# Kernel tuning notes

Hardware: AMD Instinct MI355X
Metric: run time of the kernel (lower is better)

Reference implementation:

```python
import jax, jax.numpy as jnp
import numpy as np

B, S, E, H = 4, 1024, 768, 8
HD = E // H
FF = 4 * E
SCALING = HD ** -0.5


def _layernorm(x, g, b, eps=1e-5):
    m = jnp.mean(x, axis=-1, keepdims=True)
    v = jnp.var(x, axis=-1, keepdims=True)
    return (x - m) / jnp.sqrt(v + eps) * g + b


def setup_inputs() -> dict:
    key = jax.random.key(0)
    ks = jax.random.split(key, 12)
    w = lambda k, shp: (jax.random.normal(k, shp, jnp.float32) * 0.02)
    return {
        "x": jax.random.normal(ks[0], (B, S, E), jnp.float32),
        "dist_map": jax.random.uniform(ks[1], (B, H, S, S), jnp.float32),
        "mask": jnp.zeros((B, S), jnp.int32),
        "Wq": w(ks[2], (E, E)), "bq": jnp.zeros((E,), jnp.float32),
        "Wk": w(ks[3], (E, E)), "bk": jnp.zeros((E,), jnp.float32),
        "Wv": w(ks[4], (E, E)), "bv": jnp.zeros((E,), jnp.float32),
        "Wo": w(ks[5], (E, E)), "bo": jnp.zeros((E,), jnp.float32),
        "ln1_g": jnp.ones((E,), jnp.float32), "ln1_b": jnp.zeros((E,), jnp.float32),
        "W1": w(ks[6], (FF, E)), "b1": jnp.zeros((FF,), jnp.float32),
        "W2": w(ks[7], (E, FF)), "b2": jnp.zeros((E,), jnp.float32),
        "ln2_g": jnp.ones((E,), jnp.float32), "ln2_b": jnp.zeros((E,), jnp.float32),
    }


def reference(x, dist_map, mask, Wq, bq, Wk, bk, Wv, bv, Wo, bo,
              ln1_g, ln1_b, W1, b1, W2, b2, ln2_g, ln2_b):
    # --- attention residual block (pre-norm) ---
    h = _layernorm(x, ln1_g, ln1_b)
    # NOTE: torch does .view(B, H, S, HD) directly on [B, S, E] -> pure reshape, no transpose
    q = (h @ Wq.T + bq).reshape(B, H, S, HD)
    k = (h @ Wk.T + bk).reshape(B, H, S, HD)
    v = (h @ Wv.T + bv).reshape(B, H, S, HD)
    attn_weights = jnp.einsum("bhqd,bhkd->bhqk", q, k)
    pad = mask.astype(bool)[:, None, None, :]          # [B,1,1,S]
    attn_weights = jnp.where(pad, -10000.0, attn_weights)  # mask BEFORE scaling (as in source)
    probs = jax.nn.softmax(attn_weights * SCALING, axis=-1)
    probs = (probs + dist_map) * 0.5                   # post-softmax dist bias
    ctx = jnp.einsum("bhal,bhlv->bhav", probs, v)      # [B,H,S,HD]
    ctx = ctx.transpose(0, 2, 1, 3).reshape(B, S, E)
    x1 = x + (ctx @ Wo.T + bo)
    # --- FFN residual block (pre-norm) ---
    h2 = _layernorm(x1, ln2_g, ln2_b)
    ffn = jax.nn.gelu(h2 @ W1.T + b1, approximate=False) @ W2.T + b2
    out = x1 + ffn
    return out, probs
```

## Files before the change

kernel.cpp:

```cpp
#include <hip/hip_runtime.h>
#include <math.h>

typedef unsigned short u16;
typedef u16   u16x8  __attribute__((ext_vector_type(8)));
typedef u16   u16x4  __attribute__((ext_vector_type(4)));
typedef __bf16 bf16x8 __attribute__((ext_vector_type(8)));
typedef float f32x4  __attribute__((ext_vector_type(4)));

#define SZ_BSE   3145728
#define HEADSZ   98304
#define SCALING  0.10206207261596577f

__device__ __forceinline__ u16 f2bf(float f) {
  union { float f; unsigned u; } c; c.f = f;
  unsigned u = c.u;
  return (u16)((u + 0x7fffu + ((u >> 16) & 1u)) >> 16);
}
__device__ __forceinline__ float bf2f(u16 v) {
  union { unsigned u; float f; } c; c.u = ((unsigned)v) << 16; return c.f;
}

typedef const __attribute__((address_space(1))) unsigned int* gas1_t;
typedef __attribute__((address_space(3))) unsigned int* las3_t;
__device__ __forceinline__ void gload16(const void* g, void* l) {
  __builtin_amdgcn_global_load_lds((gas1_t)g, (las3_t)l, 16, 0, 0);
}

struct CvtArgs {
  const float* src[6];
  u16* dst[6];
};
__global__ __launch_bounds__(256) void cvtall_k(CvtArgs a) {
  int bid = blockIdx.x;
  int which, base;
  if (bid < 2304)      { which = bid / 576; base = (bid - which * 576) * 1024; }
  else if (bid < 4608) { which = 4; base = (bid - 2304) * 1024; }
  else                 { which = 5; base = (bid - 4608) * 1024; }
  int i = base + threadIdx.x * 4;
  f32x4 v = *(const f32x4*)&a.src[which][i];
  u16x4 o; o[0]=f2bf(v[0]); o[1]=f2bf(v[1]); o[2]=f2bf(v[2]); o[3]=f2bf(v[3]);
  *(u16x4*)&a.dst[which][i] = o;
}

__global__ __launch_bounds__(256) void ln_k(const float* __restrict__ x,
                                            const float* __restrict__ g,
                                            const float* __restrict__ b,
                                            u16* __restrict__ out) {
  const int row = blockIdx.x;
  const float* xr = x + (long)row * 768;
  const int t = threadIdx.x;
  float v0 = xr[t], v1 = xr[t + 256], v2 = xr[t + 512];
  float s = v0 + v1 + v2, ss = v0*v0 + v1*v1 + v2*v2;
  for (int o = 32; o > 0; o >>= 1) { s += __shfl_xor(s, o); ss += __shfl_xor(ss, o); }
  __shared__ float red[8];
  int w = t >> 6;
  if ((t & 63) == 0) { red[w] = s; red[w + 4] = ss; }
  __syncthreads();
  s  = red[0] + red[1] + red[2] + red[3];
  ss = red[4] + red[5] + red[6] + red[7];
  float mean = s * (1.0f / 768.0f);
  float var  = ss * (1.0f / 768.0f) - mean * mean;
  float rstd = rsqrtf(var + 1e-5f);
  u16* orow = out + (long)row * 768;
  orow[t]       = f2bf((v0 - mean) * rstd * g[t]       + b[t]);
  orow[t + 256] = f2bf((v1 - mean) * rstd * g[t + 256] + b[t + 256]);
  orow[t + 512] = f2bf((v2 - mean) * rstd * g[t + 512] + b[t + 512]);
}

__global__ __launch_bounds__(256) void reduce_k(const float* __restrict__ p,
                                                const float* __restrict__ resid,
                                                const float* __restrict__ bias,
                                                float* __restrict__ out) {
  long i = ((long)blockIdx.x * 256 + threadIdx.x) * 4;
  f32x4 a = *(const f32x4*)&p[i];
  f32x4 b = *(const f32x4*)&p[3145728 + i];
  f32x4 c = *(const f32x4*)&p[6291456 + i];
  f32x4 r = *(const f32x4*)&resid[i];
  int cb = (int)(i % 768);
  f32x4 g = *(const f32x4*)&bias[cb];
  f32x4 o;
  o[0] = r[0] + g[0] + a[0] + b[0] + c[0];
  o[1] = r[1] + g[1] + a[1] + b[1] + c[1];
  o[2] = r[2] + g[2] + a[2] + b[2] + c[2];
  o[3] = r[3] + g[3] + a[3] + b[3] + c[3];
  *(f32x4*)&out[i] = o;
}

__global__ __launch_bounds__(512, 4)
void scores_k(const u16* __restrict__ qb, const u16* __restrict__ kb,
              const int* __restrict__ maskp, float* __restrict__ probs,
              float* __restrict__ rowsInv) {
  __shared__ float sSum[2][64];
  __shared__ u16 sFlag[1024];

  const int t = threadIdx.x;
  const int z = blockIdx.y;
  const int r0 = blockIdx.x * 64;
  const int b = z >> 3;

  {
    const int* mp = maskp + b * 1024 + t * 2;
    int2 mv = *(const int2*)mp;
    sFlag[t * 2]     = (u16)(mv.x != 0);
    sFlag[t * 2 + 1] = (u16)(mv.y != 0);
  }
  __syncthreads();

  const int lane = t & 63;
  const int w = t >> 6;
  const int rs = w & 3, ch = w >> 2;
  const int wr0 = rs * 16;
  const int lr = lane & 15, lg = lane >> 4;
  const int cbase = ch * 512;

  const u16* qh = qb + (long)z * HEADSZ;
  const u16* kh = kb + (long)z * HEADSZ;
  float* ph = probs + (long)z * 1048576;

  bf16x8 qa[3];
  {
    const u16* qr = qh + (long)(r0 + wr0 + lr) * 96 + lg * 8;
#pragma unroll
    for (int kf = 0; kf < 3; ++kf) qa[kf] = *(const bf16x8*)(qr + kf * 32);
  }

  const float neg = -10000.0f * SCALING;
  float srun[4] = {0.f, 0.f, 0.f, 0.f};

  for (int c = 0; c < 8; ++c) {
    const int c0 = cbase + c * 64;
    f32x4 a4[4] = {};
#pragma unroll
    for (int ni = 0; ni < 4; ++ni) {
      const u16* kr = kh + (long)(c0 + ni * 16 + lr) * 96 + lg * 8;
#pragma unroll
      for (int kf = 0; kf < 3; ++kf)
        a4[ni] = __builtin_amdgcn_mfma_f32_16x16x32_bf16(
            qa[kf], *(const bf16x8*)(kr + kf * 32), a4[ni], 0, 0, 0);
    }
#pragma unroll
    for (int ni = 0; ni < 4; ++ni) {
      bool fm = sFlag[c0 + ni * 16 + lr] != 0;
      float* pp = ph + (long)(r0 + wr0 + lg * 4) * 1024 + c0 + ni * 16 + lr;
#pragma unroll
      for (int r = 0; r < 4; ++r) {
        float sv = fm ? neg : a4[ni][r] * SCALING;
        float e = __expf(sv);
        srun[r] += e;
        pp[r * 1024] = e;
      }
    }
  }

#pragma unroll
  for (int r = 0; r < 4; ++r) {
    float s = srun[r];
    s += __shfl_xor(s, 1);
    s += __shfl_xor(s, 2);
    s += __shfl_xor(s, 4);
    s += __shfl_xor(s, 8);
    if (lr == 0) sSum[ch][wr0 + lg * 4 + r] = s;
  }
  __syncthreads();
  if (ch == 0 && lr == 0) {
#pragma unroll
    for (int r = 0; r < 4; ++r) {
      float iv = 1.0f / (sSum[0][wr0 + lg * 4 + r] + sSum[1][wr0 + lg * 4 + r]);
      rowsInv[(long)z * 1024 + r0 + wr0 + lg * 4 + r] = iv;
    }
  }
}

__global__ __launch_bounds__(512, 2)
void pv2_k(float* __restrict__ probs, const float* __restrict__ dist,
           const float* __restrict__ rowsInv, const u16* __restrict__ vT,
           u16* __restrict__ ctx) {
  __shared__ u16 sP[8 * 16 * 72];
  __shared__ float sX[4 * 64 * 24];

  const int t = threadIdx.x;
  const int z = blockIdx.y;
  const int r0 = blockIdx.x * 64;
  const int b = z >> 3, h = z & 7;
  const int lane = t & 63, w = t >> 6;
  const int rs = w & 3, ch = w >> 2;
  const int wr0 = rs * 16;
  const int lr = lane & 15, lg = lane >> 4;
  const int cbase = ch * 512;
  const int lrow = lane >> 2;
  const int cg = (lane & 3) * 16;
  u16* sPw = sP + w * (16 * 72);

  float* ph = probs + (long)z * 1048576;
  const float* dh = dist + (long)z * 1048576;
  const u16* vh = vT + (long)z * HEADSZ;
  const float iv = rowsInv[(long)z * 1024 + r0 + wr0 + lrow];

  f32x4 cacc[6] = {};
#pragma unroll
  for (int c = 0; c < 8; ++c) {
    const int c0 = cbase + c * 64;
    float* pp = ph + (long)(r0 + wr0 + lrow) * 1024 + c0 + cg;
    const float* dp = dh + (long)(r0 + wr0 + lrow) * 1024 + c0 + cg;
    f32x4 e0 = *(const f32x4*)pp;
    f32x4 e1 = *(const f32x4*)(pp + 4);
    f32x4 e2 = *(const f32x4*)(pp + 8);
    f32x4 e3 = *(const f32x4*)(pp + 12);
    f32x4 d0 = *(const f32x4*)dp;
    f32x4 d1 = *(const f32x4*)(dp + 4);
    f32x4 d2 = *(const f32x4*)(dp + 8);
    f32x4 d3 = *(const f32x4*)(dp + 12);
    f32x4 p0, p1, p2, p3;
#pragma unroll
    for (int j = 0; j < 4; ++j) {
      p0[j] = (e0[j] * iv + d0[j]) * 0.5f;
      p1[j] = (e1[j] * iv + d1[j]) * 0.5f;
      p2[j] = (e2[j] * iv + d2[j]) * 0.5f;
      p3[j] = (e3[j] * iv + d3[j]) * 0.5f;
    }
    *(f32x4*)pp        = p0;
    *(f32x4*)(pp + 4)  = p1;
    *(f32x4*)(pp + 8)  = p2;
    *(f32x4*)(pp + 12) = p3;
    u16x8 o0, o1;
#pragma unroll
    for (int j = 0; j < 4; ++j) {
      o0[j] = f2bf(p0[j]); o0[4 + j] = f2bf(p1[j]);
      o1[j] = f2bf(p2[j]); o1[4 + j] = f2bf(p3[j]);
    }
    *(u16x8*)&sPw[lrow * 72 + cg]     = o0;
    *(u16x8*)&sPw[lrow * 72 + cg + 8] = o1;

#pragma unroll
    for (int ks = 0; ks < 2; ++ks) {
      bf16x8 pa = *(const bf16x8*)&sPw[lr * 72 + ks * 32 + lg * 8];
      const u16* vr = vh + (long)lr * 1024 + c0 + ks * 32 + lg * 8;
#pragma unroll
      for (int n2 = 0; n2 < 6; ++n2) {
        bf16x8 vb = *(const bf16x8*)(vr + (long)n2 * 16384);
        cacc[n2] = __builtin_amdgcn_mfma_f32_16x16x32_bf16(pa, vb, cacc[n2], 0, 0, 0);
      }
    }
  }

  __syncthreads();
  if (ch == 1) {
    float* xp = sX + ((rs * 64 + lane) * 24);
#pragma unroll
    for (int n2 = 0; n2 < 6; ++n2) *(f32x4*)&xp[n2 * 4] = cacc[n2];
  }
  __syncthreads();
  if (ch == 0) {
    const float* xp = sX + ((rs * 64 + lane) * 24);
    u16* cbp = ctx + (long)b * 786432 + h * 96;
#pragma unroll
    for (int n2 = 0; n2 < 6; ++n2) {
      f32x4 xv = *(const f32x4*)&xp[n2 * 4];
      int d = n2 * 16 + lr;
#pragma unroll
      for (int r = 0; r < 4; ++r)
        cbp[(long)(r0 + wr0 + lg * 4 + r) * 768 + d] = f2bf(cacc[n2][r] + xv[r]);
    }
  }
}

enum { EPI_QKV = 0, EPI_GELU = 1, EPI_PARTIAL = 2 };

template <int EPI>
__global__ __launch_bounds__(256, 2)
void gemm_k(const u16* __restrict__ A, int lda,
            const u16* __restrict__ W, int ldw,
            void* __restrict__ Cv, long sCz, int ldc,
            const float* __restrict__ bias,
            u16* __restrict__ vt,
            int N, int K, int kchunks) {
  __shared__ u16 sA[4096];
  __shared__ u16 sB[4096];

  const int t  = threadIdx.x;
  const int kc = blockIdx.z;
  const int klen = K / kchunks;
  const int kbeg = kc * klen, kend = kbeg + klen;
  const int m0 = blockIdx.x * 128;
  const int n0 = blockIdx.y * 128;

  const int r0 = t >> 2;
  const int c0 = (t & 3) << 3;
  char* lA = (char*)sA + ((t >> 6) << 10);
  char* lB = (char*)sB + ((t >> 6) << 10);

  int bn0 = n0 + r0;      if (bn0 > N - 1) bn0 = N - 1;
  int bn1 = n0 + 64 + r0; if (bn1 > N - 1) bn1 = N - 1;
  const u16* gB0 = W + (long)bn0 * ldw + c0;
  const u16* gB1 = W + (long)bn1 * ldw + c0;
  const u16* gA0 = A + (long)(m0 + r0) * lda + c0;
  const u16* gA1 = gA0 + 64 * lda;

  const int lane = t & 63;
  const int w  = t >> 6;
  const int wm = (w >> 1) * 64, wn = (w & 1) * 64;
  const int lr = lane & 15, lg = lane >> 4;

  f32x4 acc[4][4] = {};

  for (int k0 = kbeg; k0 < kend; k0 += 32) {
    gload16(gA0 + k0, lA);
    gload16(gA1 + k0, lA + 4096);
    gload16(gB0 + k0, lB);
    gload16(gB1 + k0, lB + 4096);
    __syncthreads();

    bf16x8 aF[4], bF[4];
#pragma unroll
    for (int mi = 0; mi < 4; ++mi)
      aF[mi] = *(const bf16x8*)&sA[(wm + mi * 16 + lr) * 32 + lg * 8];
#pragma unroll
    for (int ni = 0; ni < 4; ++ni)
      bF[ni] = *(const bf16x8*)&sB[(wn + ni * 16 + lr) * 32 + lg * 8];
#pragma unroll
    for (int mi = 0; mi < 4; ++mi)
#pragma unroll
      for (int ni = 0; ni < 4; ++ni)
        acc[mi][ni] = __builtin_amdgcn_mfma_f32_16x16x32_bf16(aF[mi], bF[ni], acc[mi][ni], 0, 0, 0);
    __syncthreads();
  }

  long coff = (EPI == EPI_PARTIAL) ? (long)kc * sCz : 0;

#pragma unroll
  for (int mi = 0; mi < 4; ++mi) {
#pragma unroll
    for (int ni = 0; ni < 4; ++ni) {
      int gc = n0 + wn + ni * 16 + lr;
      if (gc >= N) continue;
      int gr0 = m0 + wm + mi * 16 + lg * 4;
#pragma unroll
      for (int r = 0; r < 4; ++r) {
        float vv = acc[mi][ni][r];
        if (EPI == EPI_QKV) {
          vv += bias[gc];
          if (gc >= 1536) {
            int c = gc - 1536;
            int row = gr0 + r, bb = row >> 10, sr = row & 1023;
            int hh = sr >> 7;
            int cd = c / 96;
            int ss = ((sr & 127) << 3) + cd;
            int dd = c - cd * 96;
            vt[(long)(bb * 8 + hh) * HEADSZ + (long)dd * 1024 + ss] = f2bf(vv);
          } else {
            int wsel = gc >= 768 ? 1 : 0;
            int c = gc - wsel * 768;
            ((u16*)Cv)[(long)wsel * 3145728 + (long)(gr0 + r) * 768 + c] = f2bf(vv);
          }
        } else if (EPI == EPI_GELU) {
          vv += bias[gc];
          vv = 0.5f * vv * (1.0f + erff(vv * 0.70710678118654752f));
          ((u16*)Cv)[coff + (long)(gr0 + r) * ldc + gc] = f2bf(vv);
        } else {
          ((float*)Cv)[coff + (long)(gr0 + r) * ldc + gc] = vv;
        }
      }
    }
  }
}

extern "C" void kernel_launch(void* const* d_in, const int* in_sizes, int n_in,
                              void* d_out, int out_size, void* d_ws, size_t ws_size,
                              hipStream_t stream) {
  (void)in_sizes; (void)n_in; (void)out_size; (void)ws_size;
  const float* x    = (const float*)d_in[0];
  const float* dist = (const float*)d_in[1];
  const int*   mask = (const int*)d_in[2];
  const float* Wq = (const float*)d_in[3];  const float* bq  = (const float*)d_in[4];
  const float* Wk = (const float*)d_in[5];  const float* bk  = (const float*)d_in[6];
  const float* Wv = (const float*)d_in[7];  const float* bv  = (const float*)d_in[8];
  const float* Wo = (const float*)d_in[9];  const float* bo  = (const float*)d_in[10];
  const float* g1 = (const float*)d_in[11]; const float* b1n = (const float*)d_in[12];
  const float* W1 = (const float*)d_in[13]; const float* b1f = (const float*)d_in[14];
  const float* W2 = (const float*)d_in[15]; const float* b2f = (const float*)d_in[16];
  const float* g2 = (const float*)d_in[17]; const float* b2n = (const float*)d_in[18];

  char* ws = (char*)d_ws;
  u16*   h    = (u16*)(ws + 0);
  u16*   ctx  = (u16*)(ws + 0);
  u16*   qk   = (u16*)(ws + 6291456);
  u16*   q    = qk;
  u16*   k    = (u16*)(ws + 12582912);
  u16*   vT   = (u16*)(ws + 25165824);
  float* part = (float*)(ws + 6291456);
  u16*   h2   = (u16*)(ws + 31457280);
  u16*   ffn1 = (u16*)(ws + 44040192);
  float* x1   = (float*)(ws + 69206016);
  u16*   wqkvb= (u16*)(ws + 81788928);
  u16*   wob  = (u16*)(ws + 85327872);
  u16*   w1b  = (u16*)(ws + 86507520);
  u16*   w2b  = (u16*)(ws + 91226112);
  float* bqkv = (float*)(ws + 95944704);
  float* rowsInv = (float*)(ws + 95953920);

  float* outp   = (float*)d_out;
  float* probs  = outp + SZ_BSE;

  CvtArgs ca;
  ca.src[0] = Wq; ca.src[1] = Wk; ca.src[2] = Wv;
  ca.src[3] = Wo; ca.src[4] = W1; ca.src[5] = W2;
  ca.dst[0] = wqkvb; ca.dst[1] = wqkvb + 589824; ca.dst[2] = wqkvb + 1179648;
  ca.dst[3] = wob;   ca.dst[4] = w1b;            ca.dst[5] = w2b;
  cvtall_k<<<6912, 256, 0, stream>>>(ca);
  hipMemcpyAsync(bqkv,        bq, 3072, hipMemcpyDeviceToDevice, stream);
  hipMemcpyAsync(bqkv + 768,  bk, 3072, hipMemcpyDeviceToDevice, stream);
  hipMemcpyAsync(bqkv + 1536, bv, 3072, hipMemcpyDeviceToDevice, stream);

  ln_k<<<4096, 256, 0, stream>>>(x, g1, b1n, h);

  gemm_k<EPI_QKV><<<dim3(32, 18, 1), 256, 0, stream>>>(
      h, 768, wqkvb, 768, qk, 0, 768, bqkv, vT, 2304, 768, 1);

  scores_k<<<dim3(16, 32), 512, 0, stream>>>(q, k, mask, probs, rowsInv);
  pv2_k<<<dim3(16, 32), 512, 0, stream>>>(probs, dist, rowsInv, vT, ctx);

  gemm_k<EPI_PARTIAL><<<dim3(32, 6, 3), 256, 0, stream>>>(
      ctx, 768, wob, 768, part, 3145728, 768, nullptr, nullptr, 768, 768, 3);
  reduce_k<<<3072, 256, 0, stream>>>(part, x, bo, x1);

  ln_k<<<4096, 256, 0, stream>>>(x1, g2, b2n, h2);

  gemm_k<EPI_GELU><<<dim3(32, 24, 1), 256, 0, stream>>>(
      h2, 768, w1b, 768, ffn1, 0, 3072, b1f, nullptr, 3072, 768, 1);

  gemm_k<EPI_PARTIAL><<<dim3(32, 6, 3), 256, 0, stream>>>(
      ffn1, 3072, w2b, 3072, part, 3145728, 768, nullptr, nullptr, 768, 3072, 3);
  reduce_k<<<3072, 256, 0, stream>>>(part, x1, b2f, outp);
}
```

Before: 341.7 us.

## Store bf16 exp scores, split probs finalize and PV, widen GEMM K-step

The scores kernel now writes unnormalized exponentials as bf16 into the upper half of each probs row, going through LDS so the global stores are coalesced. A new elementwise probs_k finalizes probs from those values and dist_map. A separate pv_k then rereads the fp32 probs and converts them to bf16 in registers before the MFMA. This is meant to cut the fp32 exp write and read traffic and to let pv_k run at higher occupancy without an LDS staging step. In exchange it adds an extra kernel launch and a second pass over probs. The GEMM now loads 64 K per barrier (double-size LDS tiles) to halve the syncs, and the N bounds clamps and checks are removed.

```diff
diff --git a/kernel.cpp b/kernel.cpp
--- a/kernel.cpp
+++ b/kernel.cpp
@@ -90,6 +90,7 @@
 void scores_k(const u16* __restrict__ qb, const u16* __restrict__ kb,
               const int* __restrict__ maskp, float* __restrict__ probs,
               float* __restrict__ rowsInv) {
+  __shared__ u16 sP[8 * 16 * 72];
   __shared__ float sSum[2][64];
   __shared__ u16 sFlag[1024];
 
@@ -112,10 +113,13 @@
   const int wr0 = rs * 16;
   const int lr = lane & 15, lg = lane >> 4;
   const int cbase = ch * 512;
+  u16* sPw = sP + w * (16 * 72);
+  const int lrow = lane >> 2;
+  const int cg = (lane & 3) * 16;
 
   const u16* qh = qb + (long)z * HEADSZ;
   const u16* kh = kb + (long)z * HEADSZ;
-  float* ph = probs + (long)z * 1048576;
+  u16* eb = (u16*)probs + (long)z * 2097152;
 
   bf16x8 qa[3];
   {
@@ -141,15 +145,19 @@
 #pragma unroll
     for (int ni = 0; ni < 4; ++ni) {
       bool fm = sFlag[c0 + ni * 16 + lr] != 0;
-      float* pp = ph + (long)(r0 + wr0 + lg * 4) * 1024 + c0 + ni * 16 + lr;
 #pragma unroll
       for (int r = 0; r < 4; ++r) {
         float sv = fm ? neg : a4[ni][r] * SCALING;
         float e = __expf(sv);
         srun[r] += e;
-        pp[r * 1024] = e;
+        sPw[(lg * 4 + r) * 72 + ni * 16 + lr] = f2bf(e);
       }
     }
+    u16x8 e0 = *(const u16x8*)&sPw[lrow * 72 + cg];
+    u16x8 e1 = *(const u16x8*)&sPw[lrow * 72 + cg + 8];
+    u16* ep = eb + (long)(r0 + wr0 + lrow) * 2048 + 1024 + c0 + cg;
+    *(u16x8*)ep       = e0;
+    *(u16x8*)(ep + 8) = e1;
   }
 
 #pragma unroll
@@ -171,86 +179,92 @@
   }
 }
 
-__global__ __launch_bounds__(512, 2)
-void pv2_k(float* __restrict__ probs, const float* __restrict__ dist,
-           const float* __restrict__ rowsInv, const u16* __restrict__ vT,
-           u16* __restrict__ ctx) {
-  __shared__ u16 sP[8 * 16 * 72];
+__global__ __launch_bounds__(256)
+void probs_k(float* __restrict__ probs, const float* __restrict__ dist,
+             const float* __restrict__ rowsInv) {
+  const long gidx = (long)blockIdx.x * 4 + (threadIdx.x >> 6);
+  const int l16 = (threadIdx.x & 63) * 16;
+  float* pr = probs + gidx * 1024 + l16;
+  const u16* er = (const u16*)(probs + gidx * 1024) + 1024 + l16;
+  const float* dr = dist + gidx * 1024 + l16;
+  const float iv = rowsInv[gidx];
+
+  u16x8 e0 = *(const u16x8*)er;
+  u16x8 e1 = *(const u16x8*)(er + 8);
+  f32x4 d0 = *(const f32x4*)dr;
+  f32x4 d1 = *(const f32x4*)(dr + 4);
+  f32x4 d2 = *(const f32x4*)(dr + 8);
+  f32x4 d3 = *(const f32x4*)(dr + 12);
+  __syncthreads();
+  f32x4 o0, o1, o2, o3;
+#pragma unroll
+  for (int j = 0; j < 4; ++j) {
+    o0[j] = (bf2f(e0[j])     * iv + d0[j]) * 0.5f;
+    o1[j] = (bf2f(e0[4 + j]) * iv + d1[j]) * 0.5f;
+    o2[j] = (bf2f(e1[j])     * iv + d2[j]) * 0.5f;
+    o3[j] = (bf2f(e1[4 + j]) * iv + d3[j]) * 0.5f;
+  }
+  *(f32x4*)pr        = o0;
+  *(f32x4*)(pr + 4)  = o1;
+  *(f32x4*)(pr + 8)  = o2;
+  *(f32x4*)(pr + 12) = o3;
+}
+
+__global__ __launch_bounds__(512, 4)
+void pv_k(const float* __restrict__ probs, const u16* __restrict__ vT,
+          u16* __restrict__ ctx) {
   __shared__ float sX[4 * 64 * 24];
-
   const int t = threadIdx.x;
   const int z = blockIdx.y;
   const int r0 = blockIdx.x * 64;
   const int b = z >> 3, h = z & 7;
   const int lane = t & 63, w = t >> 6;
-  const int rs = w & 3, ch = w >> 2;
+  const int rs = w & 3, kh = w >> 2;
   const int wr0 = rs * 16;
   const int lr = lane & 15, lg = lane >> 4;
-  const int cbase = ch * 512;
-  const int lrow = lane >> 2;
-  const int cg = (lane & 3) * 16;
-  u16* sPw = sP + w * (16 * 72);
-
-  float* ph = probs + (long)z * 1048576;
-  const float* dh = dist + (long)z * 1048576;
+
+  const float* ph = probs + (long)z * 1048576 + (long)(r0 + wr0 + lr) * 1024 + lg * 8;
   const u16* vh = vT + (long)z * HEADSZ;
-  const float iv = rowsInv[(long)z * 1024 + r0 + wr0 + lrow];
+  const int cb = kh * 512;
 
   f32x4 cacc[6] = {};
 #pragma unroll
   for (int c = 0; c < 8; ++c) {
-    const int c0 = cbase + c * 64;
-    float* pp = ph + (long)(r0 + wr0 + lrow) * 1024 + c0 + cg;
-    const float* dp = dh + (long)(r0 + wr0 + lrow) * 1024 + c0 + cg;
-    f32x4 e0 = *(const f32x4*)pp;
-    f32x4 e1 = *(const f32x4*)(pp + 4);
-    f32x4 e2 = *(const f32x4*)(pp + 8);
-    f32x4 e3 = *(const f32x4*)(pp + 12);
-    f32x4 d0 = *(const f32x4*)dp;
-    f32x4 d1 = *(const f32x4*)(dp + 4);
-    f32x4 d2 = *(const f32x4*)(dp + 8);
-    f32x4 d3 = *(const f32x4*)(dp + 12);
-    f32x4 p0, p1, p2, p3;
+    const int c0 = cb + c * 64;
+    const float* pp = ph + c0;
+    f32x4 p0 = *(const f32x4*)pp;
+    f32x4 p1 = *(const f32x4*)(pp + 4);
+    f32x4 p2 = *(const f32x4*)(pp + 32);
+    f32x4 p3 = *(const f32x4*)(pp + 36);
+    u16x8 w0, w1;
 #pragma unroll
     for (int j = 0; j < 4; ++j) {
-      p0[j] = (e0[j] * iv + d0[j]) * 0.5f;
-      p1[j] = (e1[j] * iv + d1[j]) * 0.5f;
-      p2[j] = (e2[j] * iv + d2[j]) * 0.5f;
-      p3[j] = (e3[j] * iv + d3[j]) * 0.5f;
-    }
-    *(f32x4*)pp        = p0;
-    *(f32x4*)(pp + 4)  = p1;
-    *(f32x4*)(pp + 8)  = p2;
-    *(f32x4*)(pp + 12) = p3;
-    u16x8 o0, o1;
-#pragma unroll
-    for (int j = 0; j < 4; ++j) {
-      o0[j] = f2bf(p0[j]); o0[4 + j] = f2bf(p1[j]);
-      o1[j] = f2bf(p2[j]); o1[4 + j] = f2bf(p3[j]);
-    }
-    *(u16x8*)&sPw[lrow * 72 + cg]     = o0;
-    *(u16x8*)&sPw[lrow * 72 + cg + 8] = o1;
-
-#pragma unroll
-    for (int ks = 0; ks < 2; ++ks) {
-      bf16x8 pa = *(const bf16x8*)&sPw[lr * 72 + ks * 32 + lg * 8];
-      const u16* vr = vh + (long)lr * 1024 + c0 + ks * 32 + lg * 8;
-#pragma unroll
-      for (int n2 = 0; n2 < 6; ++n2) {
-        bf16x8 vb = *(const bf16x8*)(vr + (long)n2 * 16384);
-        cacc[n2] = __builtin_amdgcn_mfma_f32_16x16x32_bf16(pa, vb, cacc[n2], 0, 0, 0);
-      }
-    }
-  }
-
-  __syncthreads();
-  if (ch == 1) {
+      w0[j] = f2bf(p0[j]); w0[4 + j] = f2bf(p1[j]);
+      w1[j] = f2bf(p2[j]); w1[4 + j] = f2bf(p3[j]);
+    }
+    bf16x8 pa0 = *(bf16x8*)&w0;
+    bf16x8 pa1 = *(bf16x8*)&w1;
+    const u16* vr0 = vh + (long)lr * 1024 + c0 + lg * 8;
+#pragma unroll
+    for (int n2 = 0; n2 < 6; ++n2) {
+      bf16x8 vb = *(const bf16x8*)(vr0 + (long)n2 * 16384);
+      cacc[n2] = __builtin_amdgcn_mfma_f32_16x16x32_bf16(pa0, vb, cacc[n2], 0, 0, 0);
+    }
+#pragma unroll
+    for (int n2 = 0; n2 < 6; ++n2) {
+      bf16x8 vb = *(const bf16x8*)(vr0 + 32 + (long)n2 * 16384);
+      cacc[n2] = __builtin_amdgcn_mfma_f32_16x16x32_bf16(pa1, vb, cacc[n2], 0, 0, 0);
+    }
+  }
+
+  __syncthreads();
+  if (kh == 1) {
     float* xp = sX + ((rs * 64 + lane) * 24);
 #pragma unroll
     for (int n2 = 0; n2 < 6; ++n2) *(f32x4*)&xp[n2 * 4] = cacc[n2];
   }
   __syncthreads();
-  if (ch == 0) {
+  if (kh == 0) {
     const float* xp = sX + ((rs * 64 + lane) * 24);
     u16* cbp = ctx + (long)b * 786432 + h * 96;
 #pragma unroll
@@ -274,8 +288,8 @@
             const float* __restrict__ bias,
             u16* __restrict__ vt,
             int N, int K, int kchunks) {
-  __shared__ u16 sA[4096];
-  __shared__ u16 sB[4096];
+  __shared__ u16 sA[8192];
+  __shared__ u16 sB[8192];
 
   const int t  = threadIdx.x;
   const int kc = blockIdx.z;
@@ -289,10 +303,8 @@
   char* lA = (char*)sA + ((t >> 6) << 10);
   char* lB = (char*)sB + ((t >> 6) << 10);
 
-  int bn0 = n0 + r0;      if (bn0 > N - 1) bn0 = N - 1;
-  int bn1 = n0 + 64 + r0; if (bn1 > N - 1) bn1 = N - 1;
-  const u16* gB0 = W + (long)bn0 * ldw + c0;
-  const u16* gB1 = W + (long)bn1 * ldw + c0;
+  const u16* gB0 = W + (long)(n0 + r0) * ldw + c0;
+  const u16* gB1 = gB0 + 64 * ldw;
   const u16* gA0 = A + (long)(m0 + r0) * lda + c0;
   const u16* gA1 = gA0 + 64 * lda;
 
@@ -303,25 +315,32 @@
 
   f32x4 acc[4][4] = {};
 
-  for (int k0 = kbeg; k0 < kend; k0 += 32) {
-    gload16(gA0 + k0, lA);
-    gload16(gA1 + k0, lA + 4096);
-    gload16(gB0 + k0, lB);
-    gload16(gB1 + k0, lB + 4096);
+  for (int k0 = kbeg; k0 < kend; k0 += 64) {
+    gload16(gA0 + k0,      lA);
+    gload16(gA1 + k0,      lA + 4096);
+    gload16(gA0 + k0 + 32, lA + 8192);
+    gload16(gA1 + k0 + 32, lA + 12288);
+    gload16(gB0 + k0,      lB);
+    gload16(gB1 + k0,      lB + 4096);
+    gload16(gB0 + k0 + 32, lB + 8192);
+    gload16(gB1 + k0 + 32, lB + 12288);
     __syncthreads();
 
-    bf16x8 aF[4], bF[4];
-#pragma unroll
-    for (int mi = 0; mi < 4; ++mi)
-      aF[mi] = *(const bf16x8*)&sA[(wm + mi * 16 + lr) * 32 + lg * 8];
-#pragma unroll
-    for (int ni = 0; ni < 4; ++ni)
-      bF[ni] = *(const bf16x8*)&sB[(wn + ni * 16 + lr) * 32 + lg * 8];
-#pragma unroll
-    for (int mi = 0; mi < 4; ++mi)
+#pragma unroll
+    for (int kk = 0; kk < 2; ++kk) {
+      bf16x8 aF[4], bF[4];
+#pragma unroll
+      for (int mi = 0; mi < 4; ++mi)
+        aF[mi] = *(const bf16x8*)&sA[kk * 4096 + (wm + mi * 16 + lr) * 32 + lg * 8];
 #pragma unroll
       for (int ni = 0; ni < 4; ++ni)
-        acc[mi][ni] = __builtin_amdgcn_mfma_f32_16x16x32_bf16(aF[mi], bF[ni], acc[mi][ni], 0, 0, 0);
+        bF[ni] = *(const bf16x8*)&sB[kk * 4096 + (wn + ni * 16 + lr) * 32 + lg * 8];
+#pragma unroll
+      for (int mi = 0; mi < 4; ++mi)
+#pragma unroll
+        for (int ni = 0; ni < 4; ++ni)
+          acc[mi][ni] = __builtin_amdgcn_mfma_f32_16x16x32_bf16(aF[mi], bF[ni], acc[mi][ni], 0, 0, 0);
+    }
     __syncthreads();
   }
 
@@ -332,7 +351,6 @@
 #pragma unroll
     for (int ni = 0; ni < 4; ++ni) {
       int gc = n0 + wn + ni * 16 + lr;
-      if (gc >= N) continue;
       int gr0 = m0 + wm + mi * 16 + lg * 4;
 #pragma unroll
       for (int r = 0; r < 4; ++r) {
@@ -417,7 +435,8 @@
       h, 768, wqkvb, 768, qk, 0, 768, bqkv, vT, 2304, 768, 1);
 
   scores_k<<<dim3(16, 32), 512, 0, stream>>>(q, k, mask, probs, rowsInv);
-  pv2_k<<<dim3(16, 32), 512, 0, stream>>>(probs, dist, rowsInv, vT, ctx);
+  probs_k<<<8192, 256, 0, stream>>>(probs, dist, rowsInv);
+  pv_k<<<dim3(16, 32), 512, 0, stream>>>(probs, vT, ctx);
 
   gemm_k<EPI_PARTIAL><<<dim3(32, 6, 3), 256, 0, stream>>>(
       ctx, 768, wob, 768, part, 3145728, 768, nullptr, nullptr, 768, 768, 3);
```

New measurement: 329.3 us. 1.04x faster.
